# Kernel optimization log

Hardware: AMD Instinct MI355X
Metric: run time of the kernel (lower is better)

The kernel has to match this reference:

```python
import jax, jax.numpy as jnp
import numpy as np

EPS_IN = 1e-5   # InstanceNorm1d eps
EPS_DM = 1e-8   # demodulation eps


def _dcoef(weight, style):
    # rsqrt(sum_i (W[o,i]*s[b,i])^2 + eps) -> [B, out]
    return jax.lax.rsqrt(jnp.einsum('oi,bi->bo', jnp.square(weight), jnp.square(style)) + EPS_DM)


def setup_inputs() -> dict:
    key = jax.random.key(0)
    ks = jax.random.split(key, 7)
    B, S, H = 8, 1024, 1024
    lim = 1.0 / np.sqrt(H)
    u = lambda k, shp: jax.random.uniform(k, shp, jnp.float32, -lim, lim)
    return {
        'x': jax.random.normal(ks[0], (B, S, H), jnp.float32),
        'q_weight': u(ks[1], (H, H)),
        'k_weight': u(ks[2], (H, H)),
        'v_weight': u(ks[3], (H, H)),
        'w_weight': u(ks[4], (H, H)),
        'u_weight': u(ks[5], (H, H)),
        'styles': jax.random.normal(ks[6], (B, 2 * H), jnp.float32) * 0.5 + 1.0,
        'num_heads': 16,
    }


def reference(x, q_weight, k_weight, v_weight, w_weight, u_weight, styles, num_heads):
    B, S, H = x.shape
    nh = num_heads
    d = H // nh
    scale = jnp.asarray(d, x.dtype) ** -0.5

    s1 = styles[:, :H]   # modulates input hidden dim of q/k/v
    s2 = styles[:, H:]   # modulates input hidden dim of w/u and v output

    # per-sample modulation + InstanceNorm over hidden dim
    x = x * s1[:, None, :]
    mu = jnp.mean(x, axis=-1, keepdims=True)
    var = jnp.mean(jnp.square(x - mu), axis=-1, keepdims=True)
    x = (x - mu) * jax.lax.rsqrt(var + EPS_IN)

    q_dc = _dcoef(q_weight, s1)  # [B,H]
    k_dc = _dcoef(k_weight, s1)
    v_dc = _dcoef(v_weight, s1)
    w_dc = _dcoef(w_weight, s2)
    u_dc = _dcoef(u_weight, s2)

    def heads(t):  # [B,S,H] -> [B,nh,S,d]
        return t.reshape(B, S, nh, d).transpose(0, 2, 1, 3)

    q = heads(jnp.einsum('bsh,oh->bso', x, q_weight) * q_dc[:, None, :])
    k = heads(jnp.einsum('bsh,oh->bso', x, k_weight) * k_dc[:, None, :])
    v_flat = jnp.einsum('bsh,oh->bso', x, v_weight) * v_dc[:, None, :] * s2[:, None, :]
    skip = v_flat
    v = heads(v_flat)

    attn = jnp.einsum('bhqd,bhkd->bhqk', q, k) * scale
    attn = jax.nn.softmax(attn, axis=-1)
    out = jnp.einsum('bhqk,bhkd->bhqd', attn, v).transpose(0, 2, 1, 3).reshape(B, S, H)

    out = jnp.einsum('bsh,oh->bso', out, w_weight) * w_dc[:, None, :]
    skip = jnp.einsum('bsh,oh->bso', skip, u_weight) * u_dc[:, None, :]
    return out + skip
```

## Files before the change

### kernel.cpp

```cpp
#include <hip/hip_runtime.h>
#include <hip/hip_bf16.h>

#define B_ 8
#define S_ 1024
#define H_ 1024
#define NH 16
#define DH 64
#define BS (B_*S_)
#define L2E 1.44269504f

typedef unsigned short u16;
typedef __attribute__((ext_vector_type(8))) short bf16x8;
typedef __attribute__((ext_vector_type(4))) float f32x4;
typedef __attribute__((ext_vector_type(4))) u16 u16x4;

#define MFMA(a,b,c) __builtin_amdgcn_mfma_f32_16x16x32_bf16((a),(b),(c),0,0,0)

__device__ __forceinline__ u16 f2bf(float f) {
  union { float f; unsigned u; } v; v.f = f;
  unsigned r = v.u + 0x7fffu + ((v.u >> 16) & 1u);
  return (u16)(r >> 16);
}

__device__ __forceinline__ unsigned packbf2(float a, float b) {
  union { __hip_bfloat162 h; unsigned u; } v;
  v.h = __float22bfloat162_rn(float2{a, b});
  return v.u;
}

__device__ __forceinline__ void gload16(const u16* g, u16* l) {
  __builtin_amdgcn_global_load_lds(
      (const __attribute__((address_space(1))) unsigned int*)g,
      (__attribute__((address_space(3))) unsigned int*)l, 16, 0, 0);
}

__global__ __launch_bounds__(256) void dcoef_kernel(
    const float* __restrict__ qw, const float* __restrict__ kw,
    const float* __restrict__ vw, const float* __restrict__ ww,
    const float* __restrict__ uw, const float* __restrict__ styles,
    float* __restrict__ dc) {
  int bi = blockIdx.x;
  int wsel = bi >> 10;
  int o = bi & 1023;
  const float* W = (wsel == 0) ? qw : (wsel == 1) ? kw : (wsel == 2) ? vw
                   : (wsel == 3) ? ww : uw;
  int soff = (wsel < 3) ? 0 : H_;
  int tid = threadIdx.x;
  float4 w4 = *(const float4*)(W + (size_t)o * H_ + tid * 4);
  float w2x = w4.x * w4.x, w2y = w4.y * w4.y, w2z = w4.z * w4.z, w2w = w4.w * w4.w;
  float acc[8];
#pragma unroll
  for (int b = 0; b < 8; b++) {
    float4 s4 = *(const float4*)(styles + (size_t)b * 2 * H_ + soff + tid * 4);
    acc[b] = w2x * s4.x * s4.x + w2y * s4.y * s4.y + w2z * s4.z * s4.z + w2w * s4.w * s4.w;
  }
#pragma unroll
  for (int off = 1; off < 64; off <<= 1)
#pragma unroll
    for (int b = 0; b < 8; b++) acc[b] += __shfl_xor(acc[b], off);
  __shared__ float red[4][8];
  int w = tid >> 6, l = tid & 63;
  if (l == 0)
#pragma unroll
    for (int b = 0; b < 8; b++) red[w][b] = acc[b];
  __syncthreads();
  if (tid < 8) {
    int b = tid;
    float v = red[0][b] + red[1][b] + red[2][b] + red[3][b];
    float r = rsqrtf(v + 1e-8f);
    if (wsel == 2) r *= styles[(size_t)b * 2 * H_ + H_ + o];
    dc[(size_t)wsel * B_ * H_ + b * H_ + o] = r;
  }
}

__global__ __launch_bounds__(256) void wconv_kernel(
    const float* __restrict__ qw, const float* __restrict__ kw,
    const float* __restrict__ vw, const float* __restrict__ ww,
    const float* __restrict__ uw, u16* __restrict__ w16) {
  int i = blockIdx.x * 256 + threadIdx.x;
  int idx = i * 4;
  int wsel = idx >> 20;
  int off = idx & (H_ * H_ - 1);
  const float* W = (wsel == 0) ? qw : (wsel == 1) ? kw : (wsel == 2) ? vw
                   : (wsel == 3) ? ww : uw;
  float4 v = *(const float4*)(W + off);
  u16x4 o = { f2bf(v.x), f2bf(v.y), f2bf(v.z), f2bf(v.w) };
  *(u16x4*)(w16 + idx) = o;
}

__global__ __launch_bounds__(256) void ln_kernel(
    const float* __restrict__ x, const float* __restrict__ styles,
    u16* __restrict__ xn) {
  int row = blockIdx.x;
  int b = row >> 10;
  int tid = threadIdx.x;
  const float4 xv = *(const float4*)(x + (size_t)row * H_ + tid * 4);
  const float4 sv = *(const float4*)(styles + (size_t)b * 2 * H_ + tid * 4);
  float v0 = xv.x * sv.x, v1 = xv.y * sv.y, v2 = xv.z * sv.z, v3 = xv.w * sv.w;
  float sum = v0 + v1 + v2 + v3;
  float sq = v0 * v0 + v1 * v1 + v2 * v2 + v3 * v3;
#pragma unroll
  for (int off = 1; off < 64; off <<= 1) {
    sum += __shfl_xor(sum, off);
    sq += __shfl_xor(sq, off);
  }
  __shared__ float rsum[4], rsq[4];
  int w = tid >> 6;
  if ((tid & 63) == 0) { rsum[w] = sum; rsq[w] = sq; }
  __syncthreads();
  sum = rsum[0] + rsum[1] + rsum[2] + rsum[3];
  sq = rsq[0] + rsq[1] + rsq[2] + rsq[3];
  float mean = sum * (1.f / H_);
  float var = sq * (1.f / H_) - mean * mean;
  float rstd = rsqrtf(var + 1e-5f);
  u16x4 o = { f2bf((v0 - mean) * rstd), f2bf((v1 - mean) * rstd),
              f2bf((v2 - mean) * rstd), f2bf((v3 - mean) * rstd) };
  *(u16x4*)(xn + (size_t)row * H_ + tid * 4) = o;
}

__device__ __forceinline__ void stage32(const u16* __restrict__ src, int K,
                                        u16* dst, int tid) {
#pragma unroll
  for (int i = 0; i < 2; i++) {
    int lrow = i * 32 + (tid >> 3);
    int ch = tid & 7;
    int lch = ch ^ (lrow & 7);
    int grow = lrow * 2 + (lch >> 2);
    gload16(src + (size_t)grow * K + (lch & 3) * 8, dst + lrow * 64 + ch * 8);
  }
}

__device__ __forceinline__ void gemm128_p3(
    const u16* __restrict__ A, const u16* __restrict__ B, int K, int NT,
    u16* ldsA, u16* ldsB, f32x4 acc[4][4]) {
  const int tid = threadIdx.x;
  const int l = tid & 63, w = tid >> 6;
  const int wm = (w >> 1) * 64, wn = (w & 1) * 64;
  const int lrow = l & 15, kc = l >> 4;
  stage32(A, K, ldsA, tid);
  stage32(B, K, ldsB, tid);
  stage32(A + 32, K, ldsA + 64 * 64, tid);
  stage32(B + 32, K, ldsB + 64 * 64, tid);
  asm volatile("s_waitcnt vmcnt(4)" ::: "memory");
  __builtin_amdgcn_s_barrier();
  int bufc = 0;
  for (int t = 0; t < NT; ++t) {
    if (t + 2 < NT) {
      int nb = bufc + 2; if (nb >= 3) nb -= 3;
      stage32(A + (size_t)(t + 2) * 32, K, ldsA + nb * (64 * 64), tid);
      stage32(B + (size_t)(t + 2) * 32, K, ldsB + nb * (64 * 64), tid);
    }
    const u16* At = ldsA + bufc * (64 * 64);
    const u16* Bt = ldsB + bufc * (64 * 64);
    bf16x8 af[4], bfr[4];
#pragma unroll
    for (int i = 0; i < 4; i++) {
      int x = wm + i * 16 + lrow;
      int ch = (((x & 1) << 2) | kc) ^ ((x >> 1) & 7);
      af[i] = *(const bf16x8*)&At[(x >> 1) * 64 + ch * 8];
    }
#pragma unroll
    for (int i = 0; i < 4; i++) {
      int x = wn + i * 16 + lrow;
      int ch = (((x & 1) << 2) | kc) ^ ((x >> 1) & 7);
      bfr[i] = *(const bf16x8*)&Bt[(x >> 1) * 64 + ch * 8];
    }
    __builtin_amdgcn_s_setprio(1);
#pragma unroll
    for (int mi = 0; mi < 4; mi++)
#pragma unroll
      for (int ni = 0; ni < 4; ni++)
        acc[mi][ni] = MFMA(af[mi], bfr[ni], acc[mi][ni]);
    __builtin_amdgcn_s_setprio(0);
    if (t + 2 < NT) {
      asm volatile("s_waitcnt vmcnt(4)" ::: "memory");
    } else if (t + 1 < NT) {
      asm volatile("s_waitcnt vmcnt(0)" ::: "memory");
    }
    __builtin_amdgcn_s_barrier();
    bufc = (bufc == 2) ? 0 : bufc + 1;
  }
}

__global__ __launch_bounds__(256, 3) void qkv_kernel(
    const u16* __restrict__ xn, const u16* __restrict__ w16,
    const float* __restrict__ dc, u16* __restrict__ Qb, u16* __restrict__ Kb,
    u16* __restrict__ VT, u16* __restrict__ vfl) {
  __shared__ u16 ldsA[3 * 64 * 64], ldsB[3 * 64 * 64];
  int bid = blockIdx.x;
  int swz = (bid & 7) * 192 + (bid >> 3);
  int bm = swz / 24, bn = swz % 24;
  f32x4 acc[4][4] = {};
  gemm128_p3(xn + (size_t)bm * 128 * H_, w16 + (size_t)bn * 128 * H_, H_, 32,
             ldsA, ldsB, acc);
  int l = threadIdx.x & 63, w = threadIdx.x >> 6;
  int wm = (w >> 1) * 64, wn = (w & 1) * 64;
  int wsel = bn >> 3;
  int col0 = (bn & 7) * 128 + wn;
  int row0 = bm * 128 + wm;
  const float* dcw = dc + (size_t)wsel * B_ * H_;
  float extra = (wsel == 0) ? 0.125f * L2E : 1.0f;
#pragma unroll
  for (int mi = 0; mi < 4; mi++) {
#pragma unroll
    for (int ni = 0; ni < 4; ni++) {
      int col = col0 + ni * 16 + (l & 15);
      int hh = col >> 6, dd = col & 63;
      int s_base = (row0 + mi * 16 + (l >> 4) * 4) & 1023;
      int b = (row0 + mi * 16 + (l >> 4) * 4) >> 10;
      float dcv = dcw[b * H_ + col] * extra;
      u16 bv[4];
#pragma unroll
      for (int rr = 0; rr < 4; rr++)
        bv[rr] = f2bf(acc[mi][ni][rr] * dcv);
      if (wsel == 0) {
#pragma unroll
        for (int rr = 0; rr < 4; rr++)
          Qb[((size_t)(b * NH + hh) * S_ + s_base + rr) * DH + dd] = bv[rr];
      } else if (wsel == 1) {
#pragma unroll
        for (int rr = 0; rr < 4; rr++)
          Kb[((size_t)(b * NH + hh) * S_ + s_base + rr) * DH + dd] = bv[rr];
      } else {
        u16x4 pv = { bv[0], bv[1], bv[2], bv[3] };
        *(u16x4*)&VT[((size_t)(b * NH + hh) * DH + dd) * S_ + s_base] = pv;
#pragma unroll
        for (int rr = 0; rr < 4; rr++)
          vfl[(size_t)(row0 + mi * 16 + (l >> 4) * 4 + rr) * H_ + col] = bv[rr];
      }
    }
  }
}

__global__ __launch_bounds__(512) void attn_kernel(
    const u16* __restrict__ Qb, const u16* __restrict__ Kb,
    const u16* __restrict__ VT, u16* __restrict__ xat) {
  __shared__ u16 ldsK[3][64 * 64];
  __shared__ u16 ldsV[3][64 * 64];
  __shared__ unsigned pls_all[8][16 * 36];
  int tid = threadIdx.x;
  int l = tid & 63, w = tid >> 6;
  int id = blockIdx.x;
  int r = id & 7, rest = id >> 3;
  int qblk = rest & 3, a = rest >> 2;
  int hl = a * 8 + r;
  int h = hl & 15, b = hl >> 4;
  int q0 = qblk * 256 + w * 32;
  const u16* Qp = Qb + ((size_t)(b * NH + h) * S_ + q0) * DH;
  const u16* Kp = Kb + (size_t)(b * NH + h) * S_ * DH;
  const u16* Vp = VT + (size_t)(b * NH + h) * DH * S_;
  unsigned* pls = pls_all[w];
  int lr = l & 15, lg = l >> 4;
  int sw = (lr & 7) << 3;
  int srow = tid >> 3, schunk = tid & 7;
  int ssw = (schunk * 8) ^ ((srow & 7) << 3);
  const u16* Ksrc = Kp + (size_t)srow * DH + ssw;
  const u16* Vsrc = Vp + (size_t)srow * S_ + ssw;
  int sdst = srow * 64 + schunk * 8;
  gload16(Ksrc, &ldsK[0][sdst]);
  gload16(Vsrc, &ldsV[0][sdst]);
  gload16(Ksrc + 64 * DH, &ldsK[1][sdst]);
  gload16(Vsrc + 64,      &ldsV[1][sdst]);
  bf16x8 qfA0 = *(const bf16x8*)(Qp + lr * 64 + lg * 8);
  bf16x8 qfA1 = *(const bf16x8*)(Qp + lr * 64 + 32 + lg * 8);
  bf16x8 qfB0 = *(const bf16x8*)(Qp + (16 + lr) * 64 + lg * 8);
  bf16x8 qfB1 = *(const bf16x8*)(Qp + (16 + lr) * 64 + 32 + lg * 8);
  f32x4 accA[4] = {}, accB[4] = {};
  float lsA = 0.f, lsB = 0.f;
  asm volatile("s_waitcnt vmcnt(2)" ::: "memory");
  __builtin_amdgcn_s_barrier();
  int cur = 0;
  for (int t = 0; t < 16; ++t) {
    if (t + 2 < 16) {
      int nb = cur + 2; if (nb >= 3) nb -= 3;
      gload16(Ksrc + (size_t)(t + 2) * 64 * DH, &ldsK[nb][sdst]);
      gload16(Vsrc + (size_t)(t + 2) * 64,      &ldsV[nb][sdst]);
    }
    const u16* Kt = &ldsK[cur][0];
    const u16* Vt = &ldsV[cur][0];
#pragma unroll
    for (int g = 0; g < 2; g++) {
      bf16x8 q0f = (g == 0) ? qfA0 : qfB0;
      bf16x8 q1f = (g == 0) ? qfA1 : qfB1;
      f32x4 st[4];
      __builtin_amdgcn_s_setprio(1);
#pragma unroll
      for (int nt = 0; nt < 4; nt++) {
        bf16x8 kf0 = *(const bf16x8*)&Kt[(nt * 16 + lr) * 64 + ((lg * 8) ^ sw)];
        bf16x8 kf1 = *(const bf16x8*)&Kt[(nt * 16 + lr) * 64 + ((32 + lg * 8) ^ sw)];
        f32x4 z = {0.f, 0.f, 0.f, 0.f};
        z = MFMA(kf0, q0f, z);
        z = MFMA(kf1, q1f, z);
        st[nt] = z;
      }
      __builtin_amdgcn_s_setprio(0);
      float rs = 0.f;
#pragma unroll
      for (int nt = 0; nt < 4; nt++)
#pragma unroll
        for (int rr = 0; rr < 4; rr++) {
          st[nt][rr] = __builtin_exp2f(st[nt][rr]);
          rs += st[nt][rr];
        }
      rs += __shfl_xor(rs, 16);
      rs += __shfl_xor(rs, 32);
      if (g == 0) lsA += rs; else lsB += rs;
      {
        unsigned* base = pls + lr * 36;
#pragma unroll
        for (int nt = 0; nt < 4; nt++) {
          uint2 pw = { packbf2(st[nt][0], st[nt][1]),
                       packbf2(st[nt][2], st[nt][3]) };
          *(uint2*)&base[nt * 8 + lg * 2] = pw;
        }
      }
      bf16x8 pb0 = *(const bf16x8*)&pls[lr * 36 + lg * 4];
      bf16x8 pb1 = *(const bf16x8*)&pls[lr * 36 + 16 + lg * 4];
      __builtin_amdgcn_s_setprio(1);
#pragma unroll
      for (int nt = 0; nt < 4; nt++) {
        bf16x8 vf0 = *(const bf16x8*)&Vt[(nt * 16 + lr) * 64 + ((lg * 8) ^ sw)];
        bf16x8 vf1 = *(const bf16x8*)&Vt[(nt * 16 + lr) * 64 + ((32 + lg * 8) ^ sw)];
        if (g == 0) {
          accA[nt] = MFMA(vf0, pb0, accA[nt]);
          accA[nt] = MFMA(vf1, pb1, accA[nt]);
        } else {
          accB[nt] = MFMA(vf0, pb0, accB[nt]);
          accB[nt] = MFMA(vf1, pb1, accB[nt]);
        }
      }
      __builtin_amdgcn_s_setprio(0);
    }
    if (t < 14) {
      asm volatile("s_waitcnt vmcnt(2)" ::: "memory");
    } else if (t == 14) {
      asm volatile("s_waitcnt vmcnt(0)" ::: "memory");
    }
    if (t < 15) __builtin_amdgcn_s_barrier();
    cur = (cur == 2) ? 0 : cur + 1;
  }
  float invA = 1.f / lsA, invB = 1.f / lsB;
#pragma unroll
  for (int nt = 0; nt < 4; nt++) {
    u16x4 oA = { f2bf(accA[nt][0] * invA), f2bf(accA[nt][1] * invA),
                 f2bf(accA[nt][2] * invA), f2bf(accA[nt][3] * invA) };
    *(u16x4*)(xat + ((size_t)(b * S_) + q0 + lr) * H_ + h * DH + nt * 16 + lg * 4) = oA;
    u16x4 oB = { f2bf(accB[nt][0] * invB), f2bf(accB[nt][1] * invB),
                 f2bf(accB[nt][2] * invB), f2bf(accB[nt][3] * invB) };
    *(u16x4*)(xat + ((size_t)(b * S_) + q0 + 16 + lr) * H_ + h * DH + nt * 16 + lg * 4) = oB;
  }
}

__global__ __launch_bounds__(256, 3) void out_kernel(
    const u16* __restrict__ xat, const u16* __restrict__ vfl,
    const u16* __restrict__ w16, const float* __restrict__ dc,
    float* __restrict__ out) {
  __shared__ u16 ldsA[3 * 64 * 64], ldsB[3 * 64 * 64];
  int bid = blockIdx.x;
  int swz = (bid & 7) * 64 + (bid >> 3);
  int bm = swz >> 3, bn = swz & 7;
  f32x4 acc[4][4] = {};
  gemm128_p3(xat + (size_t)bm * 128 * H_,
             w16 + (size_t)3 * H_ * H_ + (size_t)bn * 128 * H_, H_, 32,
             ldsA, ldsB, acc);
  int l = threadIdx.x & 63, w = threadIdx.x >> 6;
  int wm = (w >> 1) * 64, wn = (w & 1) * 64;
  int col0 = bn * 128 + wn;
  int row0 = bm * 128 + wm;
  int b = row0 >> 10;
  const float* wdc = dc + (size_t)3 * B_ * H_ + b * H_;
  const float* udc = dc + (size_t)4 * B_ * H_ + b * H_;
  float ratio[4], ud[4];
#pragma unroll
  for (int ni = 0; ni < 4; ni++) {
    int col = col0 + ni * 16 + (l & 15);
    ud[ni] = udc[col];
    ratio[ni] = wdc[col] / ud[ni];
  }
#pragma unroll
  for (int mi = 0; mi < 4; mi++)
#pragma unroll
    for (int ni = 0; ni < 4; ni++)
#pragma unroll
      for (int rr = 0; rr < 4; rr++) acc[mi][ni][rr] *= ratio[ni];
  gemm128_p3(vfl + (size_t)bm * 128 * H_,
             w16 + (size_t)4 * H_ * H_ + (size_t)bn * 128 * H_, H_, 32,
             ldsA, ldsB, acc);
#pragma unroll
  for (int mi = 0; mi < 4; mi++)
#pragma unroll
    for (int ni = 0; ni < 4; ni++) {
      int col = col0 + ni * 16 + (l & 15);
#pragma unroll
      for (int rr = 0; rr < 4; rr++) {
        int row = row0 + mi * 16 + (l >> 4) * 4 + rr;
        out[(size_t)row * H_ + col] = acc[mi][ni][rr] * ud[ni];
      }
    }
}

extern "C" void kernel_launch(void* const* d_in, const int* in_sizes, int n_in,
                              void* d_out, int out_size, void* d_ws, size_t ws_size,
                              hipStream_t stream) {
  const float* x = (const float*)d_in[0];
  const float* qw = (const float*)d_in[1];
  const float* kw = (const float*)d_in[2];
  const float* vw = (const float*)d_in[3];
  const float* ww = (const float*)d_in[4];
  const float* uw = (const float*)d_in[5];
  const float* styles = (const float*)d_in[6];
  float* out = (float*)d_out;

  char* ws = (char*)d_ws;
  size_t need = 163840 + (size_t)5 * H_ * H_ * 2 + (size_t)6 * BS * H_ * 2;
  if (ws_size < need) return;
  float* dc = (float*)ws;
  u16* w16 = (u16*)(ws + 163840);
  u16* xn  = w16 + (size_t)5 * H_ * H_;
  u16* Qb  = xn + (size_t)BS * H_;
  u16* Kb  = Qb + (size_t)BS * H_;
  u16* VT  = Kb + (size_t)BS * H_;
  u16* vfl = VT + (size_t)BS * H_;
  u16* xat = vfl + (size_t)BS * H_;

  dcoef_kernel<<<dim3(5 * H_), dim3(256), 0, stream>>>(qw, kw, vw, ww, uw, styles, dc);
  wconv_kernel<<<dim3(5120), dim3(256), 0, stream>>>(qw, kw, vw, ww, uw, w16);
  ln_kernel<<<dim3(BS), dim3(256), 0, stream>>>(x, styles, xn);
  qkv_kernel<<<dim3(1536), dim3(256), 0, stream>>>(xn, w16, dc, Qb, Kb, VT, vfl);
  attn_kernel<<<dim3(512), dim3(512), 0, stream>>>(Qb, Kb, VT, xat);
  out_kernel<<<dim3(512), dim3(256), 0, stream>>>(xat, vfl, w16, dc, out);
}
```

Measured before the change: 210.1 us.

## Enlarge QKV and output GEMM tiles to 128x256 with wave-per-column layout

Changes the shared GEMM helper from 128x128 tiles with a 2x2 wave grid to 128x256 tiles where each of four waves covers all 128 rows and 64 columns. Each wave now holds 32 accumulators and reuses each B fragment across 8 A fragments, raising MFMA work per LDS load and halving the block count for both the QKV and output projections. In exchange, register pressure and LDS per block go up, occupancy drops from 3 to 2 blocks, and the output kernel's grid shrinks to 256 blocks, which may underfill the GPU.

```diff
diff --git a/kernel.cpp b/kernel.cpp
--- a/kernel.cpp
+++ b/kernel.cpp
@@ -118,10 +118,11 @@
   *(u16x4*)(xn + (size_t)row * H_ + tid * 4) = o;
 }
 
-__device__ __forceinline__ void stage32(const u16* __restrict__ src, int K,
-                                        u16* dst, int tid) {
-#pragma unroll
-  for (int i = 0; i < 2; i++) {
+template<int NR32>
+__device__ __forceinline__ void stageT(const u16* __restrict__ src, int K,
+                                       u16* dst, int tid) {
+#pragma unroll
+  for (int i = 0; i < NR32; i++) {
     int lrow = i * 32 + (tid >> 3);
     int ch = tid & 7;
     int lch = ch ^ (lrow & 7);
@@ -130,50 +131,51 @@
   }
 }
 
-__device__ __forceinline__ void gemm128_p3(
-    const u16* __restrict__ A, const u16* __restrict__ B, int K, int NT,
-    u16* ldsA, u16* ldsB, f32x4 acc[4][4]) {
+template<int NT>
+__device__ __forceinline__ void gemm128x256(
+    const u16* __restrict__ A, const u16* __restrict__ B, int K,
+    u16* ldsA, u16* ldsB, f32x4 acc[8][4]) {
   const int tid = threadIdx.x;
   const int l = tid & 63, w = tid >> 6;
-  const int wm = (w >> 1) * 64, wn = (w & 1) * 64;
+  const int wn = w * 64;
   const int lrow = l & 15, kc = l >> 4;
-  stage32(A, K, ldsA, tid);
-  stage32(B, K, ldsB, tid);
-  stage32(A + 32, K, ldsA + 64 * 64, tid);
-  stage32(B + 32, K, ldsB + 64 * 64, tid);
-  asm volatile("s_waitcnt vmcnt(4)" ::: "memory");
+  stageT<2>(A, K, ldsA, tid);
+  stageT<4>(B, K, ldsB, tid);
+  stageT<2>(A + 32, K, ldsA + 64 * 64, tid);
+  stageT<4>(B + 32, K, ldsB + 128 * 64, tid);
+  asm volatile("s_waitcnt vmcnt(6)" ::: "memory");
   __builtin_amdgcn_s_barrier();
   int bufc = 0;
   for (int t = 0; t < NT; ++t) {
     if (t + 2 < NT) {
       int nb = bufc + 2; if (nb >= 3) nb -= 3;
-      stage32(A + (size_t)(t + 2) * 32, K, ldsA + nb * (64 * 64), tid);
-      stage32(B + (size_t)(t + 2) * 32, K, ldsB + nb * (64 * 64), tid);
+      stageT<2>(A + (size_t)(t + 2) * 32, K, ldsA + nb * (64 * 64), tid);
+      stageT<4>(B + (size_t)(t + 2) * 32, K, ldsB + nb * (128 * 64), tid);
     }
     const u16* At = ldsA + bufc * (64 * 64);
-    const u16* Bt = ldsB + bufc * (64 * 64);
-    bf16x8 af[4], bfr[4];
-#pragma unroll
-    for (int i = 0; i < 4; i++) {
-      int x = wm + i * 16 + lrow;
+    const u16* Bt = ldsB + bufc * (128 * 64);
+    bf16x8 af[8], bfr[4];
+#pragma unroll
+    for (int i = 0; i < 8; i++) {
+      int x = i * 16 + lrow;
       int ch = (((x & 1) << 2) | kc) ^ ((x >> 1) & 7);
       af[i] = *(const bf16x8*)&At[(x >> 1) * 64 + ch * 8];
     }
 #pragma unroll
     for (int i = 0; i < 4; i++) {
-      int x = wn + i * 16 + lrow;
-      int ch = (((x & 1) << 2) | kc) ^ ((x >> 1) & 7);
-      bfr[i] = *(const bf16x8*)&Bt[(x >> 1) * 64 + ch * 8];
+      int y = wn + i * 16 + lrow;
+      int ch = (((y & 1) << 2) | kc) ^ ((y >> 1) & 7);
+      bfr[i] = *(const bf16x8*)&Bt[(y >> 1) * 64 + ch * 8];
     }
     __builtin_amdgcn_s_setprio(1);
 #pragma unroll
-    for (int mi = 0; mi < 4; mi++)
+    for (int mi = 0; mi < 8; mi++)
 #pragma unroll
       for (int ni = 0; ni < 4; ni++)
         acc[mi][ni] = MFMA(af[mi], bfr[ni], acc[mi][ni]);
     __builtin_amdgcn_s_setprio(0);
     if (t + 2 < NT) {
-      asm volatile("s_waitcnt vmcnt(4)" ::: "memory");
+      asm volatile("s_waitcnt vmcnt(6)" ::: "memory");
     } else if (t + 1 < NT) {
       asm volatile("s_waitcnt vmcnt(0)" ::: "memory");
     }
@@ -182,33 +184,33 @@
   }
 }
 
-__global__ __launch_bounds__(256, 3) void qkv_kernel(
+__global__ __launch_bounds__(256, 2) void qkv_kernel(
     const u16* __restrict__ xn, const u16* __restrict__ w16,
     const float* __restrict__ dc, u16* __restrict__ Qb, u16* __restrict__ Kb,
     u16* __restrict__ VT, u16* __restrict__ vfl) {
-  __shared__ u16 ldsA[3 * 64 * 64], ldsB[3 * 64 * 64];
+  __shared__ u16 ldsA[3 * 64 * 64], ldsB[3 * 128 * 64];
   int bid = blockIdx.x;
-  int swz = (bid & 7) * 192 + (bid >> 3);
-  int bm = swz / 24, bn = swz % 24;
-  f32x4 acc[4][4] = {};
-  gemm128_p3(xn + (size_t)bm * 128 * H_, w16 + (size_t)bn * 128 * H_, H_, 32,
-             ldsA, ldsB, acc);
+  int swz = (bid & 7) * 96 + (bid >> 3);
+  int bm = swz / 12, bn = swz % 12;
+  f32x4 acc[8][4] = {};
+  gemm128x256<32>(xn + (size_t)bm * 128 * H_, w16 + (size_t)bn * 256 * H_, H_,
+                  ldsA, ldsB, acc);
   int l = threadIdx.x & 63, w = threadIdx.x >> 6;
-  int wm = (w >> 1) * 64, wn = (w & 1) * 64;
-  int wsel = bn >> 3;
-  int col0 = (bn & 7) * 128 + wn;
-  int row0 = bm * 128 + wm;
+  int lr = l & 15, lg = l >> 4;
+  int wsel = bn >> 2;
+  int col0 = (bn & 3) * 256 + w * 64;
+  int row0 = bm * 128;
   const float* dcw = dc + (size_t)wsel * B_ * H_;
   float extra = (wsel == 0) ? 0.125f * L2E : 1.0f;
 #pragma unroll
-  for (int mi = 0; mi < 4; mi++) {
+  for (int mi = 0; mi < 8; mi++) {
+    int row = row0 + mi * 16 + lg * 4;
+    int b = row >> 10, s_base = row & 1023;
 #pragma unroll
     for (int ni = 0; ni < 4; ni++) {
-      int col = col0 + ni * 16 + (l & 15);
-      int hh = col >> 6, dd = col & 63;
-      int s_base = (row0 + mi * 16 + (l >> 4) * 4) & 1023;
-      int b = (row0 + mi * 16 + (l >> 4) * 4) >> 10;
-      float dcv = dcw[b * H_ + col] * extra;
+      int cm = col0 + ni * 16 + lr;
+      int hh = cm >> 6, dd = cm & 63;
+      float dcv = dcw[b * H_ + cm] * extra;
       u16 bv[4];
 #pragma unroll
       for (int rr = 0; rr < 4; rr++)
@@ -226,7 +228,7 @@
         *(u16x4*)&VT[((size_t)(b * NH + hh) * DH + dd) * S_ + s_base] = pv;
 #pragma unroll
         for (int rr = 0; rr < 4; rr++)
-          vfl[(size_t)(row0 + mi * 16 + (l >> 4) * 4 + rr) * H_ + col] = bv[rr];
+          vfl[(size_t)(row + rr) * H_ + cm] = bv[rr];
       }
     }
   }
@@ -351,52 +353,52 @@
   }
 }
 
-__global__ __launch_bounds__(256, 3) void out_kernel(
+__global__ __launch_bounds__(256, 2) void out_kernel(
     const u16* __restrict__ xat, const u16* __restrict__ vfl,
     const u16* __restrict__ w16, const float* __restrict__ dc,
     float* __restrict__ out) {
-  __shared__ u16 ldsA[3 * 64 * 64], ldsB[3 * 64 * 64];
+  __shared__ u16 ldsA[3 * 64 * 64], ldsB[3 * 128 * 64];
   int bid = blockIdx.x;
-  int swz = (bid & 7) * 64 + (bid >> 3);
-  int bm = swz >> 3, bn = swz & 7;
-  f32x4 acc[4][4] = {};
-  gemm128_p3(xat + (size_t)bm * 128 * H_,
-             w16 + (size_t)3 * H_ * H_ + (size_t)bn * 128 * H_, H_, 32,
-             ldsA, ldsB, acc);
+  int swz = (bid & 7) * 32 + (bid >> 3);
+  int bm = swz >> 2, bn = swz & 3;
+  f32x4 acc[8][4] = {};
+  gemm128x256<32>(xat + (size_t)bm * 128 * H_,
+                  w16 + (size_t)3 * H_ * H_ + (size_t)bn * 256 * H_, H_,
+                  ldsA, ldsB, acc);
   int l = threadIdx.x & 63, w = threadIdx.x >> 6;
-  int wm = (w >> 1) * 64, wn = (w & 1) * 64;
-  int col0 = bn * 128 + wn;
-  int row0 = bm * 128 + wm;
+  int lr = l & 15, lg = l >> 4;
+  int col0 = bn * 256 + w * 64;
+  int row0 = bm * 128;
   int b = row0 >> 10;
   const float* wdc = dc + (size_t)3 * B_ * H_ + b * H_;
   const float* udc = dc + (size_t)4 * B_ * H_ + b * H_;
   float ratio[4], ud[4];
 #pragma unroll
   for (int ni = 0; ni < 4; ni++) {
-    int col = col0 + ni * 16 + (l & 15);
+    int col = col0 + ni * 16 + lr;
     ud[ni] = udc[col];
     ratio[ni] = wdc[col] / ud[ni];
   }
 #pragma unroll
-  for (int mi = 0; mi < 4; mi++)
+  for (int mi = 0; mi < 8; mi++)
 #pragma unroll
     for (int ni = 0; ni < 4; ni++)
 #pragma unroll
       for (int rr = 0; rr < 4; rr++) acc[mi][ni][rr] *= ratio[ni];
-  gemm128_p3(vfl + (size_t)bm * 128 * H_,
-             w16 + (size_t)4 * H_ * H_ + (size_t)bn * 128 * H_, H_, 32,
-             ldsA, ldsB, acc);
-#pragma unroll
-  for (int mi = 0; mi < 4; mi++)
+  gemm128x256<32>(vfl + (size_t)bm * 128 * H_,
+                  w16 + (size_t)4 * H_ * H_ + (size_t)bn * 256 * H_, H_,
+                  ldsA, ldsB, acc);
+#pragma unroll
+  for (int mi = 0; mi < 8; mi++) {
+    int row = row0 + mi * 16 + lg * 4;
 #pragma unroll
     for (int ni = 0; ni < 4; ni++) {
-      int col = col0 + ni * 16 + (l & 15);
-#pragma unroll
-      for (int rr = 0; rr < 4; rr++) {
-        int row = row0 + mi * 16 + (l >> 4) * 4 + rr;
-        out[(size_t)row * H_ + col] = acc[mi][ni][rr] * ud[ni];
-      }
-    }
+      int col = col0 + ni * 16 + lr;
+#pragma unroll
+      for (int rr = 0; rr < 4; rr++)
+        out[(size_t)(row + rr) * H_ + col] = acc[mi][ni][rr] * ud[ni];
+    }
+  }
 }
 
 extern "C" void kernel_launch(void* const* d_in, const int* in_sizes, int n_in,
@@ -426,7 +428,7 @@
   dcoef_kernel<<<dim3(5 * H_), dim3(256), 0, stream>>>(qw, kw, vw, ww, uw, styles, dc);
   wconv_kernel<<<dim3(5120), dim3(256), 0, stream>>>(qw, kw, vw, ww, uw, w16);
   ln_kernel<<<dim3(BS), dim3(256), 0, stream>>>(x, styles, xn);
-  qkv_kernel<<<dim3(1536), dim3(256), 0, stream>>>(xn, w16, dc, Qb, Kb, VT, vfl);
+  qkv_kernel<<<dim3(768), dim3(256), 0, stream>>>(xn, w16, dc, Qb, Kb, VT, vfl);
   attn_kernel<<<dim3(512), dim3(512), 0, stream>>>(Qb, Kb, VT, xat);
-  out_kernel<<<dim3(512), dim3(256), 0, stream>>>(xat, vfl, w16, dc, out);
-}
+  out_kernel<<<dim3(256), dim3(256), 0, stream>>>(xat, vfl, w16, dc, out);
+}
```

New measurement: 235.6 us. 1.12x slower.
